# Performance work log

Measured on AMD Instinct MI355X. Metric: run time of the kernel, lower is better.

Reference implementation:

```python
import jax, jax.numpy as jnp
import numpy as np

B, S, D, H = 2, 2048, 1024, 16
DH = D // H


def setup_inputs() -> dict:
    key = jax.random.key(0)
    ks = jax.random.split(key, 12)
    std = 1.0 / np.sqrt(D)
    inp = {
        "q": jax.random.normal(ks[0], (B, S, D), jnp.float32),
        "k": jax.random.normal(ks[1], (B, S, D), jnp.float32),
        "v": jax.random.normal(ks[2], (B, S, D), jnp.float32),
        "mask": jnp.tril(jnp.ones((S, S), jnp.bool_))[None, None],  # causal [1,1,S,S]
        "wq_w": jax.random.uniform(ks[3], (D, D), jnp.float32, -std, std),
        "wq_b": jax.random.uniform(ks[4], (D,), jnp.float32, -std, std),
        "wk_w": jax.random.uniform(ks[5], (D, D), jnp.float32, -std, std),
        "wk_b": jax.random.uniform(ks[6], (D,), jnp.float32, -std, std),
        "wv_w": jax.random.uniform(ks[7], (D, D), jnp.float32, -std, std),
        "wv_b": jax.random.uniform(ks[8], (D,), jnp.float32, -std, std),
        "wo_w": jax.random.uniform(ks[9], (D, D), jnp.float32, -std, std),
        "wo_b": jax.random.uniform(ks[10], (D,), jnp.float32, -std, std),
    }
    return inp


def reference(q, k, v, mask, wq_w, wq_b, wk_w, wk_b, wv_w, wv_b, wo_w, wo_b):
    b, s, d = q.shape
    dh = d // H
    scale = jnp.sqrt(jnp.asarray(dh, q.dtype))  # scale = d_model/n_heads = d_head

    def proj(x, w, bias):
        y = x @ w.T + bias
        return y.reshape(b, -1, H, dh).transpose(0, 2, 1, 3)  # [B,H,S,dh]

    Q = proj(q, wq_w, wq_b)
    K = proj(k, wk_w, wk_b)
    V = proj(v, wv_w, wv_b)

    score = jnp.einsum("bhqd,bhkd->bhqk", Q, K) / scale
    score = jnp.where(mask, score, jnp.asarray(-1e10, score.dtype))
    attn = jax.nn.softmax(score, axis=-1)
    # dropout is identity in eval mode
    y = jnp.einsum("bhqk,bhkd->bhqd", attn, V)
    y = y.transpose(0, 2, 1, 3).reshape(b, -1, d)
    y = y @ wo_w.T + wo_b
    return y, attn
```

## Files before the change

kernel.cpp:

```cpp
#include <hip/hip_runtime.h>
#include <cstdint>

#define S_LEN   2048
#define D_MODEL 1024
#define NHEAD   16
#define DHEAD   64
#define BATCH   2
#define M_ROWS  (BATCH * S_LEN)

typedef __attribute__((ext_vector_type(8))) short bf16x8;
typedef __attribute__((ext_vector_type(4))) float f32x4;

__device__ __forceinline__ unsigned short f2bf(float f) {
    union { float f; uint32_t u; } v; v.f = f;
    uint32_t u = v.u;
    return (unsigned short)((u + 0x7FFFu + ((u >> 16) & 1u)) >> 16);
}

__device__ __forceinline__ float bf2f(uint32_t u16) {
    union { uint32_t u; float f; } x; x.u = u16 << 16; return x.f;
}

__device__ __forceinline__ uint32_t cvt_pk_bf16(float a, float b) {
    uint32_t r;
    asm("v_cvt_pk_bf16_f32 %0, %1, %2" : "=v"(r) : "v"(a), "v"(b));
    return r;
}

__device__ __forceinline__ void gload_lds16(const void* g, void* l) {
    __builtin_amdgcn_global_load_lds(
        (const __attribute__((address_space(1))) void*)g,
        (__attribute__((address_space(3))) void*)l, 16, 0, 0);
}

struct CvtArgs {
    const float* src[7];
    unsigned short* dst[7];
    int n4[7];
};
__global__ __launch_bounds__(256) void cvt_all(CvtArgs a) {
    const int which = blockIdx.y;
    const int t = blockIdx.x * 256 + threadIdx.x;
    if (t >= a.n4[which]) return;
    f32x4 v = reinterpret_cast<const f32x4*>(a.src[which])[t];
    uint2 o;
    o.x = cvt_pk_bf16(v[0], v[1]);
    o.y = cvt_pk_bf16(v[2], v[3]);
    reinterpret_cast<uint2*>(a.dst[which])[t] = o;
}

template<int MODE>
__device__ __forceinline__ void gemm_body(
    unsigned short* lA, unsigned short* lB,
    const unsigned short* __restrict__ A,
    const unsigned short* __restrict__ Bw,
    const float* __restrict__ bias,
    void* __restrict__ Cout,
    int bx, int by, float prescale)
{
    constexpr int K = 1024;
    const int tid  = threadIdx.x;
    const int lane = tid & 63;
    const int w    = tid >> 6;
    const int wr   = w >> 1, wc = w & 1;
    const int g    = lane >> 4, r16 = lane & 15;
    const int brow = by * 128;
    const int bcol = bx * 128;

    f32x4 acc[4][4];
#pragma unroll
    for (int i = 0; i < 4; ++i)
#pragma unroll
        for (int j = 0; j < 4; ++j) acc[i][j] = (f32x4){0.f, 0.f, 0.f, 0.f};

    const int rA0 = tid >> 2;
    const int cc  = (tid & 3) * 8;

    for (int kk = 0; kk < K; kk += 32) {
#pragma unroll
        for (int it = 0; it < 2; ++it) {
            int r = it * 64 + rA0;
            gload_lds16(A  + (size_t)(brow + r) * K + kk + cc, &lA[r * 32 + cc]);
            gload_lds16(Bw + (size_t)(bcol + r) * K + kk + cc, &lB[r * 32 + cc]);
        }
        __syncthreads();
        bf16x8 af[4], bfr[4];
#pragma unroll
        for (int i = 0; i < 4; ++i)
            af[i] = *reinterpret_cast<const bf16x8*>(&lA[(wr * 64 + i * 16 + r16) * 32 + g * 8]);
#pragma unroll
        for (int j = 0; j < 4; ++j)
            bfr[j] = *reinterpret_cast<const bf16x8*>(&lB[(wc * 64 + j * 16 + r16) * 32 + g * 8]);
#pragma unroll
        for (int i = 0; i < 4; ++i)
#pragma unroll
            for (int j = 0; j < 4; ++j)
                acc[i][j] = __builtin_amdgcn_mfma_f32_16x16x32_bf16(af[i], bfr[j], acc[i][j], 0, 0, 0);
        __syncthreads();
    }

#pragma unroll
    for (int i = 0; i < 4; ++i) {
#pragma unroll
        for (int j = 0; j < 4; ++j) {
            const int n = bcol + wc * 64 + j * 16 + r16;
#pragma unroll
            for (int rr = 0; rr < 4; ++rr) {
                const int m = brow + wr * 64 + i * 16 + g * 4 + rr;
                float val = acc[i][j][rr];
                if (MODE == 0) {
                    val = (val + bias[n]) * prescale;
                    int b = m >> 11, s = m & 2047;
                    int h = n >> 6,  d = n & 63;
                    ((unsigned short*)Cout)[(((size_t)(b * NHEAD + h)) * S_LEN + s) * DHEAD + d] = f2bf(val);
                } else if (MODE == 1) {
                    val += bias[m];
                    int h = m >> 6,  d = m & 63;
                    int b = n >> 11, s = n & 2047;
                    ((unsigned short*)Cout)[(((size_t)(b * NHEAD + h)) * DHEAD + d) * S_LEN + s] = f2bf(val);
                } else {
                    val += bias[n];
                    ((float*)Cout)[(size_t)m * D_MODEL + n] = val;
                }
            }
        }
    }
}

__global__ __launch_bounds__(256) void proj_all(
    const unsigned short* qb, const unsigned short* wqb, const float* wq_b, unsigned short* Qhp,
    const unsigned short* kb, const unsigned short* wkb, const float* wk_b, unsigned short* Khp,
    const unsigned short* vb, const unsigned short* wvb, const float* wv_b, unsigned short* Vtp,
    float qscale)
{
    __shared__ unsigned short lA[128 * 32];
    __shared__ unsigned short lB[128 * 32];
    const int bid = blockIdx.x;
    const int z = bid >> 8, t = bid & 255;
    if (z == 0)
        gemm_body<0>(lA, lB, qb, wqb, wq_b, Qhp, t & 7, t >> 3, qscale);
    else if (z == 1)
        gemm_body<0>(lA, lB, kb, wkb, wk_b, Khp, t & 7, t >> 3, 1.0f);
    else
        gemm_body<1>(lA, lB, wvb, vb, wv_b, Vtp, t & 31, t >> 5, 1.0f);
}

__global__ __launch_bounds__(512, 2) void attn_ctx_kernel(
    const unsigned short* __restrict__ Qh,
    const unsigned short* __restrict__ Kh,
    const unsigned short* __restrict__ Vt,
    float* __restrict__ stats,
    unsigned short* __restrict__ ctx)
{
    __shared__ unsigned short ldsK[2][64 * 64];
    __shared__ unsigned short ldsV[2][64 * 64];
    __shared__ unsigned short pS[8][16 * 72];

    const int tid  = threadIdx.x;
    const int lane = tid & 63;
    const int w    = tid >> 6;
    const int g    = lane >> 4, r16 = lane & 15;
    const int wg   = w & 3;
    const int grp  = w >> 2;

    const int lid = blockIdx.x;
    const int xcd = lid & 7;
    const int rest = lid >> 3;
    const int bh  = xcd * 4 + (rest >> 3);
    const int ii  = rest & 7;
    const int b   = bh >> 4, h = bh & 15;

    const unsigned short* Kp = Kh + (size_t)bh * S_LEN * DHEAD;
    const unsigned short* Vp = Vt + (size_t)bh * DHEAD * S_LEN;

    const int srow = tid >> 3;
    const int scol = (tid & 7) * 16;
    const int sswz = scol ^ ((srow & 7) << 4);
    const int rsw  = (r16 & 7) << 4;

    unsigned short* pl = pS[w];

    for (int pp = 0; pp < 2; ++pp) {
        const int p  = pp == 0 ? ii : 15 - ii;
        const int qh = 16 + p;
        const int ql = 15 - p;
        const int qtile = grp == 0 ? qh : ql;
        const int qw    = qtile * 64 + wg * 16;
        const int qrel  = wg * 16 + r16;
        const int myN   = qtile;

        const unsigned short* Qp = Qh + ((size_t)bh * S_LEN + qw) * DHEAD;
        bf16x8 qf[2];
#pragma unroll
        for (int d2 = 0; d2 < 2; ++d2)
            qf[d2] = *reinterpret_cast<const bf16x8*>(Qp + (size_t)r16 * DHEAD + d2 * 32 + g * 8);

        auto stageKV = [&](int kt, int buf) {
            gload_lds16((const char*)Kp + (size_t)(kt * 64 + srow) * 128 + sswz,
                        (char*)ldsK[buf] + tid * 16);
            gload_lds16((const char*)Vp + (size_t)srow * (S_LEN * 2) + (size_t)kt * 128 + sswz,
                        (char*)ldsV[buf] + tid * 16);
        };

        float l_run = 0.f;
        f32x4 of[4];
#pragma unroll
        for (int nt = 0; nt < 4; ++nt) of[nt] = (f32x4){0, 0, 0, 0};

        int buf = 0;
        stageKV(0, 0);
        __syncthreads();
        for (int t = 0; t <= qh; ++t) {
            if (t < qh) stageKV(t + 1, buf ^ 1);
            if (t <= myN) {
                const bool masked = (t == myN);
                bf16x8 kf[8];
#pragma unroll
                for (int d2 = 0; d2 < 2; ++d2)
#pragma unroll
                    for (int nt = 0; nt < 4; ++nt)
                        kf[d2 * 4 + nt] = *reinterpret_cast<const bf16x8*>(
                            (const char*)ldsK[buf] + (nt * 16 + r16) * 128 + ((d2 * 64 + g * 16) ^ rsw));
                f32x4 sf[4];
#pragma unroll
                for (int nt = 0; nt < 4; ++nt) sf[nt] = (f32x4){0, 0, 0, 0};
                __builtin_amdgcn_s_setprio(1);
#pragma unroll
                for (int d2 = 0; d2 < 2; ++d2)
#pragma unroll
                    for (int nt = 0; nt < 4; ++nt)
                        sf[nt] = __builtin_amdgcn_mfma_f32_16x16x32_bf16(kf[d2 * 4 + nt], qf[d2], sf[nt], 0, 0, 0);
                __builtin_amdgcn_s_setprio(0);
                float sum = 0.f;
#pragma unroll
                for (int nt = 0; nt < 4; ++nt)
#pragma unroll
                    for (int rr = 0; rr < 4; ++rr) {
                        float e = __builtin_amdgcn_exp2f(sf[nt][rr]);
                        if (masked && (nt * 16 + g * 4 + rr > qrel)) e = 0.f;
                        sf[nt][rr] = e;
                        sum += e;
                    }
                l_run += sum;
#pragma unroll
                for (int nt = 0; nt < 4; ++nt) {
                    uint2 pk2;
                    pk2.x = cvt_pk_bf16(sf[nt][0], sf[nt][1]);
                    pk2.y = cvt_pk_bf16(sf[nt][2], sf[nt][3]);
                    *reinterpret_cast<uint2*>(&pl[r16 * 72 + nt * 16 + g * 4]) = pk2;
                }
                __builtin_amdgcn_wave_barrier();
                __builtin_amdgcn_s_setprio(1);
#pragma unroll
                for (int kh = 0; kh < 2; ++kh) {
                    bf16x8 pa = *reinterpret_cast<const bf16x8*>(&pl[r16 * 72 + kh * 32 + g * 8]);
#pragma unroll
                    for (int nt = 0; nt < 4; ++nt) {
                        bf16x8 vf = *reinterpret_cast<const bf16x8*>(
                            (const char*)ldsV[buf] + (nt * 16 + r16) * 128 + ((kh * 64 + g * 16) ^ rsw));
                        of[nt] = __builtin_amdgcn_mfma_f32_16x16x32_bf16(vf, pa, of[nt], 0, 0, 0);
                    }
                }
                __builtin_amdgcn_s_setprio(0);
            }
            __syncthreads();
            buf ^= 1;
        }

        float lx = l_run;
        lx += __shfl_xor(lx, 16);
        lx += __shfl_xor(lx, 32);
        const float mprime = __builtin_amdgcn_logf(lx);
        if (lane < 16)
            stats[(size_t)bh * S_LEN + qw + r16] = mprime;

        const float inv = 1.f / lx;
        const size_t crow = ((size_t)b * S_LEN + qw + r16) * D_MODEL + h * DHEAD;
#pragma unroll
        for (int nt = 0; nt < 4; ++nt) {
            uint2 pk2;
            pk2.x = cvt_pk_bf16(of[nt][0] * inv, of[nt][1] * inv);
            pk2.y = cvt_pk_bf16(of[nt][2] * inv, of[nt][3] * inv);
            *reinterpret_cast<uint2*>(&ctx[crow + nt * 16 + g * 4]) = pk2;
        }
        __syncthreads();
    }
}

__global__ __launch_bounds__(256) void fused_out(
    const unsigned short* __restrict__ ctx,
    const unsigned short* __restrict__ wob,
    const float* __restrict__ wo_b,
    float* __restrict__ yout,
    const unsigned short* __restrict__ Qh,
    const unsigned short* __restrict__ Kh,
    const float* __restrict__ stats,
    float* __restrict__ attn_out)
{
    __shared__ unsigned short lds[128 * 32 * 2];
    const int bid = blockIdx.x;
    if (bid < 256) {
        gemm_body<2>(lds, lds + 128 * 32, ctx, wob, wo_b, yout, bid & 7, bid >> 3, 1.0f);
        return;
    }

    const int tid  = threadIdx.x;
    const int lane = tid & 63;
    const int w    = tid >> 6;
    const int g    = lane >> 4, r16 = lane & 15;
    const int rl   = lane >> 4;
    const int c4   = (lane & 15) * 4;

    const int pid = bid - 256;
    const int xcd = pid & 7;
    const int cid = pid >> 3;
    const int bh  = xcd * 4 + cid / 528;
    int t = cid % 528;
    int qt = (int)((sqrtf(8.f * t + 1.f) - 1.f) * 0.5f);
    while ((qt + 1) * (qt + 2) / 2 <= t) ++qt;
    while (qt * (qt + 1) / 2 > t) --qt;
    const int kt = t - qt * (qt + 1) / 2;

    float* abase = attn_out + (size_t)bh * S_LEN * S_LEN;

    if (kt < qt) {
        float* dstZ = abase + (size_t)(kt * 64) * S_LEN + qt * 64;
        const f32x4 z4 = (f32x4){0.f, 0.f, 0.f, 0.f};
#pragma unroll
        for (int i = 0; i < 4; ++i) {
            const int r = i * 4 + rl + w * 16;
            __builtin_nontemporal_store(z4,
                reinterpret_cast<f32x4*>(dstZ + (size_t)r * S_LEN + c4));
        }
    }

    const int qw = qt * 64 + w * 16;
    float* dst0 = abase + (size_t)qw * S_LEN + kt * 64;

    const unsigned short* Qp = Qh + ((size_t)bh * S_LEN + qw) * DHEAD;
    const unsigned short* Kp = Kh + ((size_t)bh * S_LEN + kt * 64) * DHEAD;

    bf16x8 qf[2];
#pragma unroll
    for (int d2 = 0; d2 < 2; ++d2)
        qf[d2] = *reinterpret_cast<const bf16x8*>(Qp + (size_t)r16 * DHEAD + d2 * 32 + g * 8);
    bf16x8 kf[8];
#pragma unroll
    for (int d2 = 0; d2 < 2; ++d2)
#pragma unroll
        for (int nt = 0; nt < 4; ++nt)
            kf[d2 * 4 + nt] = *reinterpret_cast<const bf16x8*>(
                Kp + (size_t)(nt * 16 + r16) * DHEAD + d2 * 32 + g * 8);
    const float mpr = stats[(size_t)bh * S_LEN + qw + r16];

    f32x4 sf[4];
#pragma unroll
    for (int nt = 0; nt < 4; ++nt) sf[nt] = (f32x4){0, 0, 0, 0};
    __builtin_amdgcn_s_setprio(1);
#pragma unroll
    for (int d2 = 0; d2 < 2; ++d2)
#pragma unroll
        for (int nt = 0; nt < 4; ++nt)
            sf[nt] = __builtin_amdgcn_mfma_f32_16x16x32_bf16(kf[d2 * 4 + nt], qf[d2], sf[nt], 0, 0, 0);
    __builtin_amdgcn_s_setprio(0);

    const bool masked = (kt == qt);
    const int qrel = w * 16 + r16;
    unsigned short* pl = lds + w * (16 * 72);
#pragma unroll
    for (int nt = 0; nt < 4; ++nt) {
#pragma unroll
        for (int rr = 0; rr < 4; ++rr) {
            float p = __builtin_amdgcn_exp2f(sf[nt][rr] - mpr);
            if (masked && (nt * 16 + g * 4 + rr > qrel)) p = 0.f;
            sf[nt][rr] = p;
        }
        uint2 pk2;
        pk2.x = cvt_pk_bf16(sf[nt][0], sf[nt][1]);
        pk2.y = cvt_pk_bf16(sf[nt][2], sf[nt][3]);
        *reinterpret_cast<uint2*>(&pl[r16 * 72 + nt * 16 + g * 4]) = pk2;
    }
    __builtin_amdgcn_wave_barrier();
#pragma unroll
    for (int i = 0; i < 4; ++i) {
        const int r = i * 4 + rl;
        uint2 dpk = *reinterpret_cast<const uint2*>(&pl[r * 72 + c4]);
        f32x4 o;
        o[0] = bf2f(dpk.x & 0xffffu);
        o[1] = bf2f(dpk.x >> 16);
        o[2] = bf2f(dpk.y & 0xffffu);
        o[3] = bf2f(dpk.y >> 16);
        __builtin_nontemporal_store(o, reinterpret_cast<f32x4*>(dst0 + (size_t)r * S_LEN + c4));
    }
}

extern "C" void kernel_launch(void* const* d_in, const int* in_sizes, int n_in,
                              void* d_out, int out_size, void* d_ws, size_t ws_size,
                              hipStream_t stream)
{
    const float* q    = (const float*)d_in[0];
    const float* k    = (const float*)d_in[1];
    const float* v    = (const float*)d_in[2];
    const float* wq_w = (const float*)d_in[4];
    const float* wq_b = (const float*)d_in[5];
    const float* wk_w = (const float*)d_in[6];
    const float* wk_b = (const float*)d_in[7];
    const float* wv_w = (const float*)d_in[8];
    const float* wv_b = (const float*)d_in[9];
    const float* wo_w = (const float*)d_in[10];
    const float* wo_b = (const float*)d_in[11];

    char* ws = (char*)d_ws;
    const size_t MB = 1024 * 1024;
    unsigned short* qb  = (unsigned short*)(ws + 0 * MB);
    unsigned short* kb  = (unsigned short*)(ws + 8 * MB);
    unsigned short* vb  = (unsigned short*)(ws + 16 * MB);
    unsigned short* wqb = (unsigned short*)(ws + 24 * MB);
    unsigned short* wkb = (unsigned short*)(ws + 26 * MB);
    unsigned short* wvb = (unsigned short*)(ws + 28 * MB);
    unsigned short* wob = (unsigned short*)(ws + 30 * MB);
    unsigned short* Qhp = (unsigned short*)(ws + 32 * MB);
    unsigned short* Khp = (unsigned short*)(ws + 40 * MB);
    unsigned short* Vtp = (unsigned short*)(ws + 48 * MB);
    unsigned short* ctx = (unsigned short*)(ws + 56 * MB);
    float* stats = (float*)(ws + 0 * MB);

    float* yout = (float*)d_out;
    float* attn = yout + (size_t)M_ROWS * D_MODEL;

    CvtArgs ca;
    ca.src[0] = q;    ca.dst[0] = qb;  ca.n4[0] = M_ROWS * D_MODEL / 4;
    ca.src[1] = k;    ca.dst[1] = kb;  ca.n4[1] = M_ROWS * D_MODEL / 4;
    ca.src[2] = v;    ca.dst[2] = vb;  ca.n4[2] = M_ROWS * D_MODEL / 4;
    ca.src[3] = wq_w; ca.dst[3] = wqb; ca.n4[3] = D_MODEL * D_MODEL / 4;
    ca.src[4] = wk_w; ca.dst[4] = wkb; ca.n4[4] = D_MODEL * D_MODEL / 4;
    ca.src[5] = wv_w; ca.dst[5] = wvb; ca.n4[5] = D_MODEL * D_MODEL / 4;
    ca.src[6] = wo_w; ca.dst[6] = wob; ca.n4[6] = D_MODEL * D_MODEL / 4;
    cvt_all<<<dim3((M_ROWS * D_MODEL / 4 + 255) / 256, 7), dim3(256), 0, stream>>>(ca);

    const float qscale = 0.125f * 1.44269504088896340736f;
    proj_all<<<dim3(768), dim3(256), 0, stream>>>(
        qb, wqb, wq_b, Qhp,
        kb, wkb, wk_b, Khp,
        vb, wvb, wv_b, Vtp, qscale);

    attn_ctx_kernel<<<dim3(256), dim3(512), 0, stream>>>(Qhp, Khp, Vtp, stats, ctx);

    fused_out<<<dim3(256 + 16896), dim3(256), 0, stream>>>(
        ctx, wob, wo_b, yout, Qhp, Khp, stats, attn);
}
```

Baseline: 226.8 us.

## Process full query-tile rows per block in attention-probability writer

Replaces the one-block-per-(q,k) tile grid of 16896 blocks with one block per (head, query tile), which loops over all causal key tiles and then zero-fills the masked upper region of its own rows. The aim is to cut block launch and scheduling overhead and to keep Q fragments in registers across key tiles. The trade-off is that triangular work becomes load-imbalanced across blocks (qt ranges 0..31) with only 1024 blocks. The zero-fill now writes contiguous row segments instead of transposed tiles.

```diff
diff --git a/kernel.cpp b/kernel.cpp
--- a/kernel.cpp
+++ b/kernel.cpp
@@ -313,84 +313,80 @@
 
     const int pid = bid - 256;
     const int xcd = pid & 7;
-    const int cid = pid >> 3;
-    const int bh  = xcd * 4 + cid / 528;
-    int t = cid % 528;
-    int qt = (int)((sqrtf(8.f * t + 1.f) - 1.f) * 0.5f);
-    while ((qt + 1) * (qt + 2) / 2 <= t) ++qt;
-    while (qt * (qt + 1) / 2 > t) --qt;
-    const int kt = t - qt * (qt + 1) / 2;
-
-    float* abase = attn_out + (size_t)bh * S_LEN * S_LEN;
-
-    if (kt < qt) {
-        float* dstZ = abase + (size_t)(kt * 64) * S_LEN + qt * 64;
-        const f32x4 z4 = (f32x4){0.f, 0.f, 0.f, 0.f};
-#pragma unroll
-        for (int i = 0; i < 4; ++i) {
-            const int r = i * 4 + rl + w * 16;
-            __builtin_nontemporal_store(z4,
-                reinterpret_cast<f32x4*>(dstZ + (size_t)r * S_LEN + c4));
-        }
-    }
-
-    const int qw = qt * 64 + w * 16;
-    float* dst0 = abase + (size_t)qw * S_LEN + kt * 64;
+    const int rest = pid >> 3;
+    const int bh  = xcd * 4 + (rest >> 5);
+    const int qt  = rest & 31;
+
+    const int qw   = qt * 64 + w * 16;
+    const int qrel = w * 16 + r16;
+    float* rowbase = attn_out + (size_t)bh * S_LEN * S_LEN + (size_t)qw * S_LEN;
 
     const unsigned short* Qp = Qh + ((size_t)bh * S_LEN + qw) * DHEAD;
-    const unsigned short* Kp = Kh + ((size_t)bh * S_LEN + kt * 64) * DHEAD;
+    const unsigned short* Kp = Kh + (size_t)bh * S_LEN * DHEAD;
 
     bf16x8 qf[2];
 #pragma unroll
     for (int d2 = 0; d2 < 2; ++d2)
         qf[d2] = *reinterpret_cast<const bf16x8*>(Qp + (size_t)r16 * DHEAD + d2 * 32 + g * 8);
-    bf16x8 kf[8];
-#pragma unroll
-    for (int d2 = 0; d2 < 2; ++d2)
-#pragma unroll
-        for (int nt = 0; nt < 4; ++nt)
-            kf[d2 * 4 + nt] = *reinterpret_cast<const bf16x8*>(
-                Kp + (size_t)(nt * 16 + r16) * DHEAD + d2 * 32 + g * 8);
     const float mpr = stats[(size_t)bh * S_LEN + qw + r16];
 
-    f32x4 sf[4];
-#pragma unroll
-    for (int nt = 0; nt < 4; ++nt) sf[nt] = (f32x4){0, 0, 0, 0};
-    __builtin_amdgcn_s_setprio(1);
-#pragma unroll
-    for (int d2 = 0; d2 < 2; ++d2)
-#pragma unroll
-        for (int nt = 0; nt < 4; ++nt)
-            sf[nt] = __builtin_amdgcn_mfma_f32_16x16x32_bf16(kf[d2 * 4 + nt], qf[d2], sf[nt], 0, 0, 0);
-    __builtin_amdgcn_s_setprio(0);
-
-    const bool masked = (kt == qt);
-    const int qrel = w * 16 + r16;
     unsigned short* pl = lds + w * (16 * 72);
-#pragma unroll
-    for (int nt = 0; nt < 4; ++nt) {
-#pragma unroll
-        for (int rr = 0; rr < 4; ++rr) {
-            float p = __builtin_amdgcn_exp2f(sf[nt][rr] - mpr);
-            if (masked && (nt * 16 + g * 4 + rr > qrel)) p = 0.f;
-            sf[nt][rr] = p;
-        }
-        uint2 pk2;
-        pk2.x = cvt_pk_bf16(sf[nt][0], sf[nt][1]);
-        pk2.y = cvt_pk_bf16(sf[nt][2], sf[nt][3]);
-        *reinterpret_cast<uint2*>(&pl[r16 * 72 + nt * 16 + g * 4]) = pk2;
-    }
-    __builtin_amdgcn_wave_barrier();
-#pragma unroll
-    for (int i = 0; i < 4; ++i) {
-        const int r = i * 4 + rl;
-        uint2 dpk = *reinterpret_cast<const uint2*>(&pl[r * 72 + c4]);
-        f32x4 o;
-        o[0] = bf2f(dpk.x & 0xffffu);
-        o[1] = bf2f(dpk.x >> 16);
-        o[2] = bf2f(dpk.y & 0xffffu);
-        o[3] = bf2f(dpk.y >> 16);
-        __builtin_nontemporal_store(o, reinterpret_cast<f32x4*>(dst0 + (size_t)r * S_LEN + c4));
+
+    for (int kt = 0; kt <= qt; ++kt) {
+        bf16x8 kf[8];
+#pragma unroll
+        for (int d2 = 0; d2 < 2; ++d2)
+#pragma unroll
+            for (int nt = 0; nt < 4; ++nt)
+                kf[d2 * 4 + nt] = *reinterpret_cast<const bf16x8*>(
+                    Kp + (size_t)(kt * 64 + nt * 16 + r16) * DHEAD + d2 * 32 + g * 8);
+        f32x4 sf[4];
+#pragma unroll
+        for (int nt = 0; nt < 4; ++nt) sf[nt] = (f32x4){0, 0, 0, 0};
+        __builtin_amdgcn_s_setprio(1);
+#pragma unroll
+        for (int d2 = 0; d2 < 2; ++d2)
+#pragma unroll
+            for (int nt = 0; nt < 4; ++nt)
+                sf[nt] = __builtin_amdgcn_mfma_f32_16x16x32_bf16(kf[d2 * 4 + nt], qf[d2], sf[nt], 0, 0, 0);
+        __builtin_amdgcn_s_setprio(0);
+
+        const bool masked = (kt == qt);
+#pragma unroll
+        for (int nt = 0; nt < 4; ++nt) {
+#pragma unroll
+            for (int rr = 0; rr < 4; ++rr) {
+                float p = __builtin_amdgcn_exp2f(sf[nt][rr] - mpr);
+                if (masked && (nt * 16 + g * 4 + rr > qrel)) p = 0.f;
+                sf[nt][rr] = p;
+            }
+            uint2 pk2;
+            pk2.x = cvt_pk_bf16(sf[nt][0], sf[nt][1]);
+            pk2.y = cvt_pk_bf16(sf[nt][2], sf[nt][3]);
+            *reinterpret_cast<uint2*>(&pl[r16 * 72 + nt * 16 + g * 4]) = pk2;
+        }
+        __builtin_amdgcn_wave_barrier();
+        float* dst0 = rowbase + kt * 64;
+#pragma unroll
+        for (int i = 0; i < 4; ++i) {
+            const int r = i * 4 + rl;
+            uint2 dpk = *reinterpret_cast<const uint2*>(&pl[r * 72 + c4]);
+            f32x4 o;
+            o[0] = bf2f(dpk.x & 0xffffu);
+            o[1] = bf2f(dpk.x >> 16);
+            o[2] = bf2f(dpk.y & 0xffffu);
+            o[3] = bf2f(dpk.y >> 16);
+            __builtin_nontemporal_store(o, reinterpret_cast<f32x4*>(dst0 + (size_t)r * S_LEN + c4));
+        }
+        __builtin_amdgcn_wave_barrier();
+    }
+
+    const int z0 = (qt + 1) * 64;
+    const f32x4 z4 = (f32x4){0.f, 0.f, 0.f, 0.f};
+    for (int r = 0; r < 16; ++r) {
+        float* dst = rowbase + (size_t)r * S_LEN;
+        for (int c = z0 + lane * 4; c < S_LEN; c += 256)
+            __builtin_nontemporal_store(z4, reinterpret_cast<f32x4*>(dst + c));
     }
 }
 
@@ -446,6 +442,6 @@
 
     attn_ctx_kernel<<<dim3(256), dim3(512), 0, stream>>>(Qhp, Khp, Vtp, stats, ctx);
 
-    fused_out<<<dim3(256 + 16896), dim3(256), 0, stream>>>(
+    fused_out<<<dim3(256 + 1024), dim3(256), 0, stream>>>(
         ctx, wob, wo_b, yout, Qhp, Khp, stats, attn);
 }
```

After: 253.3 us. 11.7% more time.
